# Performance work log

Hardware: AMD Instinct MI355X
Metric: run time of the kernel (lower is better)

The kernel has to match this reference:

```python
import jax, jax.numpy as jnp
import numpy as np

N_HEADS = 16
ROPE_DIMS = 64


def _rope_tables(T, rd):
    # freqs: 1 / 10000^(arange(0, rd, 2)/rd), shape [rd//2]
    freqs = 1.0 / (10000.0 ** (np.arange(0, rd, 2, dtype=np.float32) / np.float32(rd)))
    ang = np.outer(np.arange(T, dtype=np.float32), freqs)  # [T, rd//2]
    return jnp.asarray(np.cos(ang)), jnp.asarray(np.sin(ang))


def _apply_rope(x, cos, sin, rd):
    # x: [B, H, T, D]; rotate-half style on first rd dims
    x_rope, x_pass = x[..., :rd], x[..., rd:]
    x1, x2 = x_rope[..., : rd // 2], x_rope[..., rd // 2 :]
    c = cos[None, None]  # [1,1,T,rd//2]
    s = sin[None, None]
    x_rot = jnp.concatenate([x1 * c - x2 * s, x2 * c + x1 * s], axis=-1)
    return jnp.concatenate([x_rot, x_pass], axis=-1)


def setup_inputs() -> dict:
    key = jax.random.key(0)
    k1, k2, k3 = jax.random.split(key, 3)
    B, T, C = 32, 512, 2048
    x = jax.random.normal(k1, (B, T, C), dtype=jnp.float32)
    w_qkv = jax.random.normal(k2, (3 * C, C), dtype=jnp.float32) * 0.02
    w_out = jax.random.normal(k3, (C, C), dtype=jnp.float32) * 0.02
    return {"x": x, "w_qkv": w_qkv, "w_out": w_out}


def reference(x, w_qkv, w_out):
    B, T, C = x.shape
    H = N_HEADS
    D = C // H
    # fused QKV projection: F.linear(x, w) = x @ w.T
    qkv = jnp.einsum('btc,fc->btf', x, w_qkv).reshape(B, T, 3, H, D)
    q = jnp.transpose(qkv[:, :, 0], (0, 2, 1, 3))  # [B,H,T,D]
    k = jnp.transpose(qkv[:, :, 1], (0, 2, 1, 3))
    v = jnp.transpose(qkv[:, :, 2], (0, 2, 1, 3))
    cos, sin = _rope_tables(T, ROPE_DIMS)
    q = _apply_rope(q, cos, sin, ROPE_DIMS)
    k = _apply_rope(k, cos, sin, ROPE_DIMS)
    # causal SDPA
    scale = 1.0 / jnp.sqrt(jnp.asarray(D, dtype=x.dtype))
    scores = jnp.einsum('bhqd,bhkd->bhqk', q, k) * scale
    causal = jnp.tril(jnp.ones((T, T), dtype=bool))
    scores = jnp.where(causal[None, None], scores, jnp.finfo(scores.dtype).min)
    attn = jax.nn.softmax(scores, axis=-1)
    y = jnp.einsum('bhqk,bhkd->bhqd', attn, v)
    y = jnp.transpose(y, (0, 2, 1, 3)).reshape(B, T, C)
    return jnp.einsum('btc,fc->btf', y, w_out)
```

## Files before the change

kernel.cpp:

```cpp
#include <hip/hip_runtime.h>


typedef __bf16 bf16x8 __attribute__((ext_vector_type(8)));
typedef float floatx4 __attribute__((ext_vector_type(4)));

__device__ __forceinline__ unsigned short f2bf(float f) {
  union { float f; unsigned u; } v; v.f = f;
  unsigned r = v.u + 0x7FFFu + ((v.u >> 16) & 1u);
  return (unsigned short)(r >> 16);
}
__device__ __forceinline__ float bf2f(unsigned short h) {
  union { unsigned u; float f; } v; v.u = ((unsigned)h) << 16; return v.f;
}

__device__ __forceinline__ void load_lds16(const void* g, void* l) {
  __builtin_amdgcn_global_load_lds((__attribute__((address_space(1))) void*)g,
                                   (__attribute__((address_space(3))) void*)l,
                                   16, 0, 0);
}

#define BARRIER() asm volatile("s_barrier" ::: "memory")
#define VMCNT6()  asm volatile("s_waitcnt vmcnt(6)" ::: "memory")
#define VMCNT0()  asm volatile("s_waitcnt vmcnt(0)" ::: "memory")
#define LGKM0()   asm volatile("s_waitcnt lgkmcnt(0)" ::: "memory")

__global__ void rope_tables(float* __restrict__ cost, float* __restrict__ sint) {
  int i = blockIdx.x * 256 + threadIdx.x;
  if (i >= 512 * 32) return;
  int t = i >> 5, f = i & 31;
  float e = -(float)(2 * f) / 64.0f;
  float freq = powf(10000.0f, e);
  float ang = (float)t * freq;
  cost[i] = cosf(ang);
  sint[i] = sinf(ang);
}

__global__ void cast_bf16(const float* __restrict__ in,
                          unsigned short* __restrict__ out, int n8) {
  int i = blockIdx.x * 256 + threadIdx.x;
  if (i >= n8) return;
  float4 a = ((const float4*)in)[2 * i];
  float4 b = ((const float4*)in)[2 * i + 1];
  union { uint4 v; unsigned short u[8]; } o;
  o.u[0] = f2bf(a.x); o.u[1] = f2bf(a.y); o.u[2] = f2bf(a.z); o.u[3] = f2bf(a.w);
  o.u[4] = f2bf(b.x); o.u[5] = f2bf(b.y); o.u[6] = f2bf(b.z); o.u[7] = f2bf(b.w);
  ((uint4*)out)[i] = o.v;
}

template <int OUT_BF16>
__global__ __launch_bounds__(512, 2) void gemm256(
    const unsigned short* __restrict__ A, const unsigned short* __restrict__ Bt,
    void* __restrict__ Cout, int M, int N, int K) {
  __shared__ __align__(16) unsigned short As[2][16384];
  __shared__ __align__(16) unsigned short Bs[2][16384];

  const int tid = threadIdx.x;
  const int nbx = gridDim.x;
  const int nwg = nbx * gridDim.y;
  const int lin = blockIdx.y * nbx + blockIdx.x;
  const int swz = (lin & 7) * (nwg >> 3) + (lin >> 3);
  const int bm = swz / nbx, bn = swz % nbx;

  const int w = tid >> 6, l = tid & 63;
  const int wm = w >> 2, wn = w & 3;
  const int quad = l >> 4, cl = l & 15;
  const int xs0 = ((0 + quad) ^ (cl & 7)) << 3;
  const int xs1 = ((4 + quad) ^ (cl & 7)) << 3;
  const int aoff = (wm * 128 + cl) * 64;
  const int boff = (wn * 64 + cl) * 64;

  const int srow = tid >> 3;
  const int lc = (tid & 7) ^ (srow & 7);
  const unsigned short* Ag = A + (size_t)(bm * 256 + srow) * K + lc * 8;
  const unsigned short* Bg = Bt + (size_t)(bn * 256 + srow) * K + lc * 8;

  auto stageA = [&](int q, int h, int k0) {
    const unsigned short* src = Ag + (size_t)(h * 128) * K + k0;
    unsigned short* dst = &As[q][0] + h * 8192 + tid * 8;
    load_lds16(src, dst);
    load_lds16(src + (size_t)64 * K, dst + 4096);
  };
  auto stageB = [&](int q, int h, int k0) {
    const unsigned short* src = Bg + (size_t)(h * 128) * K + k0;
    unsigned short* dst = &Bs[q][0] + h * 8192 + tid * 8;
    load_lds16(src, dst);
    load_lds16(src + (size_t)64 * K, dst + 4096);
  };

  floatx4 acc[8][4] = {};
  const int NT = K >> 6;

  stageA(0, 0, 0);  stageA(0, 1, 0);  stageB(0, 0, 0);  stageB(0, 1, 0);
  stageA(1, 0, 64); stageA(1, 1, 64); stageB(1, 0, 64);
  VMCNT6();
  BARRIER();

  for (int t = 0; t < NT; ++t) {
    const int q = t & 1;
    const unsigned short* pA = &As[q][0] + aoff;
    const unsigned short* pB = &Bs[q][0] + boff;
    const int k2 = (t + 2) << 6;
    const bool s2 = (t + 2) < NT;

    bf16x8 a[8][2], b[2][2];
#pragma unroll
    for (int mi = 0; mi < 8; ++mi) {
      a[mi][0] = *(const bf16x8*)(pA + mi * 1024 + xs0);
      a[mi][1] = *(const bf16x8*)(pA + mi * 1024 + xs1);
    }
#pragma unroll
    for (int ni = 0; ni < 2; ++ni) {
      b[ni][0] = *(const bf16x8*)(pB + ni * 1024 + xs0);
      b[ni][1] = *(const bf16x8*)(pB + ni * 1024 + xs1);
    }
    if (t + 1 < NT) stageB(q ^ 1, 1, (t + 1) << 6);
    BARRIER();
    __builtin_amdgcn_s_setprio(1);
#pragma unroll
    for (int mi = 0; mi < 4; ++mi)
#pragma unroll
      for (int ni = 0; ni < 2; ++ni)
#pragma unroll
        for (int ks = 0; ks < 2; ++ks)
          acc[mi][ni] = __builtin_amdgcn_mfma_f32_16x16x32_bf16(
              a[mi][ks], b[ni][ks], acc[mi][ni], 0, 0, 0);
    __builtin_amdgcn_s_setprio(0);
    LGKM0();
    BARRIER();
    if (s2) stageA(q, 0, k2);
    BARRIER();
    __builtin_amdgcn_s_setprio(1);
#pragma unroll
    for (int mi = 4; mi < 8; ++mi)
#pragma unroll
      for (int ni = 0; ni < 2; ++ni)
#pragma unroll
        for (int ks = 0; ks < 2; ++ks)
          acc[mi][ni] = __builtin_amdgcn_mfma_f32_16x16x32_bf16(
              a[mi][ks], b[ni][ks], acc[mi][ni], 0, 0, 0);
    __builtin_amdgcn_s_setprio(0);
    BARRIER();
#pragma unroll
    for (int ni = 0; ni < 2; ++ni) {
      b[ni][0] = *(const bf16x8*)(pB + (ni + 2) * 1024 + xs0);
      b[ni][1] = *(const bf16x8*)(pB + (ni + 2) * 1024 + xs1);
    }
    if (s2) stageA(q, 1, k2);
    BARRIER();
    __builtin_amdgcn_s_setprio(1);
#pragma unroll
    for (int mi = 0; mi < 4; ++mi)
#pragma unroll
      for (int ni = 0; ni < 2; ++ni)
#pragma unroll
        for (int ks = 0; ks < 2; ++ks)
          acc[mi][ni + 2] = __builtin_amdgcn_mfma_f32_16x16x32_bf16(
              a[mi][ks], b[ni][ks], acc[mi][ni + 2], 0, 0, 0);
    __builtin_amdgcn_s_setprio(0);
    BARRIER();
    if (s2) stageB(q, 0, k2);
    BARRIER();
    __builtin_amdgcn_s_setprio(1);
#pragma unroll
    for (int mi = 4; mi < 8; ++mi)
#pragma unroll
      for (int ni = 0; ni < 2; ++ni)
#pragma unroll
        for (int ks = 0; ks < 2; ++ks)
          acc[mi][ni + 2] = __builtin_amdgcn_mfma_f32_16x16x32_bf16(
              a[mi][ks], b[ni][ks], acc[mi][ni + 2], 0, 0, 0);
    __builtin_amdgcn_s_setprio(0);
    if (t < NT - 2) { VMCNT6(); } else { VMCNT0(); }
    BARRIER();
  }

#pragma unroll
  for (int mi = 0; mi < 8; ++mi)
#pragma unroll
    for (int ni = 0; ni < 4; ++ni)
#pragma unroll
      for (int r = 0; r < 4; ++r) {
        const int gm = bm * 256 + wm * 128 + mi * 16 + quad * 4 + r;
        const int gn = bn * 256 + wn * 64 + ni * 16 + cl;
        const float v = acc[mi][ni][r];
        if (OUT_BF16)
          ((unsigned short*)Cout)[(size_t)gm * N + gn] = f2bf(v);
        else
          ((float*)Cout)[(size_t)gm * N + gn] = v;
      }
}

__global__ __launch_bounds__(256) void attn_kernel(
    const unsigned short* __restrict__ qkv, const float* __restrict__ cost,
    const float* __restrict__ sint, unsigned short* __restrict__ y) {
  __shared__ __align__(16) unsigned short Qs[64][136];
  __shared__ __align__(16) unsigned short Ks[64][136];
  __shared__ __align__(16) unsigned short VTs[128][64];
  __shared__ __align__(16) unsigned short Ps[4][16][72];

  const int bh = blockIdx.x, qt = blockIdx.y;
  const int b = bh >> 4, h = bh & 15;
  const int tid = threadIdx.x, w = tid >> 6, l = tid & 63;
  const int quad = l >> 4, cl = l & 15;
  const float scale = 0.08838834764831845f * 1.4426950408889634f;

  {
    const int r = tid >> 2, j = tid & 3;
    const int tg = qt * 64 + r;
    const unsigned short* qrow = qkv + (size_t)(b * 512 + tg) * 6144 + h * 128;
    union { uint4 v; unsigned short u[8]; } c1, c2, p1, p2, o1, o2, o3, o4;
    c1.v = *(const uint4*)(qrow + j * 8);
    c2.v = *(const uint4*)(qrow + j * 8 + 32);
    p1.v = *(const uint4*)(qrow + 64 + j * 16);
    p2.v = *(const uint4*)(qrow + 64 + j * 16 + 8);
#pragma unroll
    for (int jj = 0; jj < 8; ++jj) {
      int d = j * 8 + jj;
      float c = cost[tg * 32 + d], s = sint[tg * 32 + d];
      float x1 = bf2f(c1.u[jj]), x2 = bf2f(c2.u[jj]);
      o1.u[jj] = f2bf((x1 * c - x2 * s) * scale);
      o2.u[jj] = f2bf((x2 * c + x1 * s) * scale);
      o3.u[jj] = f2bf(bf2f(p1.u[jj]) * scale);
      o4.u[jj] = f2bf(bf2f(p2.u[jj]) * scale);
    }
    *(uint4*)&Qs[r][j * 8]          = o1.v;
    *(uint4*)&Qs[r][j * 8 + 32]     = o2.v;
    *(uint4*)&Qs[r][64 + j * 16]     = o3.v;
    *(uint4*)&Qs[r][64 + j * 16 + 8] = o4.v;
  }

  floatx4 o[8] = {};
  float m_i[4] = {-__builtin_inff(), -__builtin_inff(), -__builtin_inff(),
                  -__builtin_inff()};
  float l_i[4] = {0.f, 0.f, 0.f, 0.f};

  for (int ktile = 0; ktile <= qt; ++ktile) {
    __syncthreads();
    {
      const int r = tid >> 2, j = tid & 3;
      const int tg = ktile * 64 + r;
      const unsigned short* krow =
          qkv + (size_t)(b * 512 + tg) * 6144 + 2048 + h * 128;
      union { uint4 v; unsigned short u[8]; } c1, c2, p1, p2, o1, o2;
      c1.v = *(const uint4*)(krow + j * 8);
      c2.v = *(const uint4*)(krow + j * 8 + 32);
      p1.v = *(const uint4*)(krow + 64 + j * 16);
      p2.v = *(const uint4*)(krow + 64 + j * 16 + 8);
#pragma unroll
      for (int jj = 0; jj < 8; ++jj) {
        int d = j * 8 + jj;
        float c = cost[tg * 32 + d], s = sint[tg * 32 + d];
        float x1 = bf2f(c1.u[jj]), x2 = bf2f(c2.u[jj]);
        o1.u[jj] = f2bf(x1 * c - x2 * s);
        o2.u[jj] = f2bf(x2 * c + x1 * s);
      }
      *(uint4*)&Ks[r][j * 8]          = o1.v;
      *(uint4*)&Ks[r][j * 8 + 32]     = o2.v;
      *(uint4*)&Ks[r][64 + j * 16]     = p1.v;
      *(uint4*)&Ks[r][64 + j * 16 + 8] = p2.v;
    }
    {
      const int rowg = tid >> 5;
      const int colg = tid & 31;
      const int kk0 = rowg * 8, d0 = colg * 4;
      const unsigned short* vbase = qkv +
          (size_t)(b * 512 + ktile * 64 + kk0) * 6144 + 4096 + h * 128 + d0;
      uint2 rv[8];
#pragma unroll
      for (int rr = 0; rr < 8; ++rr)
        rv[rr] = *(const uint2*)(vbase + (size_t)rr * 6144);
#pragma unroll
      for (int c = 0; c < 4; ++c) {
        const int d = d0 + c;
        unsigned out[4];
#pragma unroll
        for (int p = 0; p < 4; ++p) {
          unsigned ua = ((const unsigned*)&rv[2 * p])[c >> 1];
          unsigned ub = ((const unsigned*)&rv[2 * p + 1])[c >> 1];
          unsigned lo = (c & 1) ? (ua >> 16) : (ua & 0xffffu);
          unsigned hi = (c & 1) ? (ub >> 16) : (ub & 0xffffu);
          out[p] = lo | (hi << 16);
        }
        *(uint4*)&VTs[d][(rowg ^ (d & 7)) << 3] = *(uint4*)out;
      }
    }
    __syncthreads();

    floatx4 s[4] = {};
#pragma unroll
    for (int kc = 0; kc < 4; ++kc) {
      bf16x8 aq = *(const bf16x8*)(&Qs[w * 16 + cl][kc * 32 + quad * 8]);
#pragma unroll
      for (int nt = 0; nt < 4; ++nt) {
        bf16x8 bk = *(const bf16x8*)(&Ks[nt * 16 + cl][kc * 32 + quad * 8]);
        s[nt] = __builtin_amdgcn_mfma_f32_16x16x32_bf16(aq, bk, s[nt], 0, 0, 0);
      }
    }
    if (ktile == qt) {
#pragma unroll
      for (int nt = 0; nt < 4; ++nt)
#pragma unroll
        for (int r = 0; r < 4; ++r) {
          int qrow_l = w * 16 + quad * 4 + r;
          int kcol_l = nt * 16 + cl;
          if (kcol_l > qrow_l) s[nt][r] = -__builtin_inff();
        }
    }
#pragma unroll
    for (int r = 0; r < 4; ++r) {
      float mx = fmaxf(fmaxf(s[0][r], s[1][r]), fmaxf(s[2][r], s[3][r]));
      mx = fmaxf(mx, __shfl_xor(mx, 1));
      mx = fmaxf(mx, __shfl_xor(mx, 2));
      mx = fmaxf(mx, __shfl_xor(mx, 4));
      mx = fmaxf(mx, __shfl_xor(mx, 8));
      float mn = fmaxf(m_i[r], mx);
      float a = exp2f(m_i[r] - mn);
      float rs = 0.f;
#pragma unroll
      for (int nt = 0; nt < 4; ++nt) {
        float p = exp2f(s[nt][r] - mn);
        s[nt][r] = p;
        rs += p;
      }
      rs += __shfl_xor(rs, 1);
      rs += __shfl_xor(rs, 2);
      rs += __shfl_xor(rs, 4);
      rs += __shfl_xor(rs, 8);
      l_i[r] = l_i[r] * a + rs;
      m_i[r] = mn;
#pragma unroll
      for (int nt2 = 0; nt2 < 8; ++nt2) o[nt2][r] *= a;
#pragma unroll
      for (int nt = 0; nt < 4; ++nt)
        Ps[w][quad * 4 + r][nt * 16 + cl] = f2bf(s[nt][r]);
    }
    __syncthreads();

#pragma unroll
    for (int kc2 = 0; kc2 < 2; ++kc2) {
      bf16x8 ap = *(const bf16x8*)(&Ps[w][cl][kc2 * 32 + quad * 8]);
#pragma unroll
      for (int nt2 = 0; nt2 < 8; ++nt2) {
        bf16x8 bv = *(const bf16x8*)(
            &VTs[nt2 * 16 + cl][((kc2 * 4 + quad) ^ (cl & 7)) << 3]);
        o[nt2] = __builtin_amdgcn_mfma_f32_16x16x32_bf16(ap, bv, o[nt2], 0, 0, 0);
      }
    }
  }

#pragma unroll
  for (int r = 0; r < 4; ++r) {
    float inv = 1.0f / l_i[r];
    size_t row =
        (size_t)(b * 512 + qt * 64 + w * 16 + quad * 4 + r) * 2048 + h * 128;
#pragma unroll
    for (int nt2 = 0; nt2 < 8; ++nt2)
      y[row + nt2 * 16 + cl] = f2bf(o[nt2][r] * inv);
  }
}

extern "C" void kernel_launch(void* const* d_in, const int* in_sizes, int n_in,
                              void* d_out, int out_size, void* d_ws,
                              size_t ws_size, hipStream_t stream) {
  const float* x = (const float*)d_in[0];
  const float* wqkv = (const float*)d_in[1];
  const float* wout = (const float*)d_in[2];
  float* out = (float*)d_out;

  char* ws = (char*)d_ws;
  float* cost = (float*)ws;            ws += (size_t)512 * 32 * 4;
  float* sint = (float*)ws;            ws += (size_t)512 * 32 * 4;
  unsigned short* xb = (unsigned short*)ws;    ws += (size_t)16384 * 2048 * 2;
  unsigned short* wqkvb = (unsigned short*)ws; ws += (size_t)6144 * 2048 * 2;
  unsigned short* woutb = (unsigned short*)ws; ws += (size_t)2048 * 2048 * 2;
  unsigned short* qkvb = (unsigned short*)ws;  ws += (size_t)16384 * 6144 * 2;
  unsigned short* yb = (unsigned short*)ws;    ws += (size_t)16384 * 2048 * 2;

  rope_tables<<<dim3(64), dim3(256), 0, stream>>>(cost, sint);
  cast_bf16<<<dim3(16384), dim3(256), 0, stream>>>(x, xb, 33554432 / 8);
  cast_bf16<<<dim3(6144), dim3(256), 0, stream>>>(wqkv, wqkvb, 12582912 / 8);
  cast_bf16<<<dim3(2048), dim3(256), 0, stream>>>(wout, woutb, 4194304 / 8);
  gemm256<1><<<dim3(24, 64), dim3(512), 0, stream>>>(xb, wqkvb, (void*)qkvb,
                                                     16384, 6144, 2048);
  attn_kernel<<<dim3(512, 8), dim3(256), 0, stream>>>(qkvb, cost, sint, yb);
  gemm256<0><<<dim3(8, 64), dim3(512), 0, stream>>>(yb, woutb, (void*)out,
                                                    16384, 2048, 2048);
}
```

Measured before the change: 981.4 us.

## Split A fragment loads and reorder MFMA quadrants to interleave LDS reads

Restructures the GEMM inner loop so A fragments load in two halves (a0, a1), with the second half read from LDS after the first quadrant of MFMAs instead of all upfront. MFMA quadrants now run in a serpentine order (a0b0, a1b0, a1b1, a0b1), and the stageA(q,1)/stageB(q,0) global-to-LDS prefetches merge into one phase. This removes the explicit lgkmcnt(0) wait and spreads LDS reads between MFMA bursts to lower register pressure and hide LDS latency. It risks sync correctness because the buffer-reuse ordering relative to the barriers has changed.

```diff
diff --git a/kernel.cpp b/kernel.cpp
--- a/kernel.cpp
+++ b/kernel.cpp
@@ -22,7 +22,6 @@
 #define BARRIER() asm volatile("s_barrier" ::: "memory")
 #define VMCNT6()  asm volatile("s_waitcnt vmcnt(6)" ::: "memory")
 #define VMCNT0()  asm volatile("s_waitcnt vmcnt(0)" ::: "memory")
-#define LGKM0()   asm volatile("s_waitcnt lgkmcnt(0)" ::: "memory")
 
 __global__ void rope_tables(float* __restrict__ cost, float* __restrict__ sint) {
   int i = blockIdx.x * 256 + threadIdx.x;
@@ -102,16 +101,16 @@
     const int k2 = (t + 2) << 6;
     const bool s2 = (t + 2) < NT;
 
-    bf16x8 a[8][2], b[2][2];
-#pragma unroll
-    for (int mi = 0; mi < 8; ++mi) {
-      a[mi][0] = *(const bf16x8*)(pA + mi * 1024 + xs0);
-      a[mi][1] = *(const bf16x8*)(pA + mi * 1024 + xs1);
+    bf16x8 a0[4][2], a1[4][2], b0[2][2], b1[2][2];
+#pragma unroll
+    for (int mi = 0; mi < 4; ++mi) {
+      a0[mi][0] = *(const bf16x8*)(pA + mi * 1024 + xs0);
+      a0[mi][1] = *(const bf16x8*)(pA + mi * 1024 + xs1);
     }
 #pragma unroll
     for (int ni = 0; ni < 2; ++ni) {
-      b[ni][0] = *(const bf16x8*)(pB + ni * 1024 + xs0);
-      b[ni][1] = *(const bf16x8*)(pB + ni * 1024 + xs1);
+      b0[ni][0] = *(const bf16x8*)(pB + ni * 1024 + xs0);
+      b0[ni][1] = *(const bf16x8*)(pB + ni * 1024 + xs1);
     }
     if (t + 1 < NT) stageB(q ^ 1, 1, (t + 1) << 6);
     BARRIER();
@@ -123,29 +122,45 @@
 #pragma unroll
         for (int ks = 0; ks < 2; ++ks)
           acc[mi][ni] = __builtin_amdgcn_mfma_f32_16x16x32_bf16(
-              a[mi][ks], b[ni][ks], acc[mi][ni], 0, 0, 0);
+              a0[mi][ks], b0[ni][ks], acc[mi][ni], 0, 0, 0);
     __builtin_amdgcn_s_setprio(0);
-    LGKM0();
-    BARRIER();
+    BARRIER();
+#pragma unroll
+    for (int mi = 0; mi < 4; ++mi) {
+      a1[mi][0] = *(const bf16x8*)(pA + (mi + 4) * 1024 + xs0);
+      a1[mi][1] = *(const bf16x8*)(pA + (mi + 4) * 1024 + xs1);
+    }
+    BARRIER();
+    __builtin_amdgcn_s_setprio(1);
+#pragma unroll
+    for (int mi = 0; mi < 4; ++mi)
+#pragma unroll
+      for (int ni = 0; ni < 2; ++ni)
+#pragma unroll
+        for (int ks = 0; ks < 2; ++ks)
+          acc[mi + 4][ni] = __builtin_amdgcn_mfma_f32_16x16x32_bf16(
+              a1[mi][ks], b0[ni][ks], acc[mi + 4][ni], 0, 0, 0);
+    __builtin_amdgcn_s_setprio(0);
+    BARRIER();
+#pragma unroll
+    for (int ni = 0; ni < 2; ++ni) {
+      b1[ni][0] = *(const bf16x8*)(pB + (ni + 2) * 1024 + xs0);
+      b1[ni][1] = *(const bf16x8*)(pB + (ni + 2) * 1024 + xs1);
+    }
     if (s2) stageA(q, 0, k2);
     BARRIER();
     __builtin_amdgcn_s_setprio(1);
 #pragma unroll
-    for (int mi = 4; mi < 8; ++mi)
+    for (int mi = 0; mi < 4; ++mi)
 #pragma unroll
       for (int ni = 0; ni < 2; ++ni)
 #pragma unroll
         for (int ks = 0; ks < 2; ++ks)
-          acc[mi][ni] = __builtin_amdgcn_mfma_f32_16x16x32_bf16(
-              a[mi][ks], b[ni][ks], acc[mi][ni], 0, 0, 0);
+          acc[mi + 4][ni + 2] = __builtin_amdgcn_mfma_f32_16x16x32_bf16(
+              a1[mi][ks], b1[ni][ks], acc[mi + 4][ni + 2], 0, 0, 0);
     __builtin_amdgcn_s_setprio(0);
     BARRIER();
-#pragma unroll
-    for (int ni = 0; ni < 2; ++ni) {
-      b[ni][0] = *(const bf16x8*)(pB + (ni + 2) * 1024 + xs0);
-      b[ni][1] = *(const bf16x8*)(pB + (ni + 2) * 1024 + xs1);
-    }
-    if (s2) stageA(q, 1, k2);
+    if (s2) { stageA(q, 1, k2); stageB(q, 0, k2); }
     BARRIER();
     __builtin_amdgcn_s_setprio(1);
 #pragma unroll
@@ -155,20 +170,7 @@
 #pragma unroll
         for (int ks = 0; ks < 2; ++ks)
           acc[mi][ni + 2] = __builtin_amdgcn_mfma_f32_16x16x32_bf16(
-              a[mi][ks], b[ni][ks], acc[mi][ni + 2], 0, 0, 0);
-    __builtin_amdgcn_s_setprio(0);
-    BARRIER();
-    if (s2) stageB(q, 0, k2);
-    BARRIER();
-    __builtin_amdgcn_s_setprio(1);
-#pragma unroll
-    for (int mi = 4; mi < 8; ++mi)
-#pragma unroll
-      for (int ni = 0; ni < 2; ++ni)
-#pragma unroll
-        for (int ks = 0; ks < 2; ++ks)
-          acc[mi][ni + 2] = __builtin_amdgcn_mfma_f32_16x16x32_bf16(
-              a[mi][ks], b[ni][ks], acc[mi][ni + 2], 0, 0, 0);
+              a0[mi][ks], b1[ni][ks], acc[mi][ni + 2], 0, 0, 0);
     __builtin_amdgcn_s_setprio(0);
     if (t < NT - 2) { VMCNT6(); } else { VMCNT0(); }
     BARRIER();
```

Result: faster. 948.8 us (-3.3%).
